# Optimization experiments

Measured on AMD Instinct MI355X. Metric: run time of the kernel, lower is better.

The kernel has to match this reference:

```python
import jax, jax.numpy as jnp
import numpy as np
import math

B, S, D, H, DH = 2, 4096, 1024, 16, 64
CHUNK, RNDS, NBUCK, MLP = 128, 2, 64, 4096


def setup_inputs() -> dict:
    key = jax.random.key(0)
    ks = jax.random.split(key, 8)
    return {
        "inputs": jax.random.normal(ks[0], (B, S, D), jnp.float32),
        "ln1_scale": jnp.ones((D,), jnp.float32),
        "ln1_bias": jnp.zeros((D,), jnp.float32),
        "w_qk": jax.random.normal(ks[1], (D, H, DH), jnp.float32) * 0.02,
        "w_v": jax.random.normal(ks[2], (D, H, DH), jnp.float32) * 0.02,
        "w_out": jax.random.normal(ks[3], (H, DH, D), jnp.float32) * 0.02,
        "rotations": jax.random.normal(ks[4], (DH, RNDS, NBUCK // 2), jnp.float32),
        "ln2_scale": jnp.ones((D,), jnp.float32),
        "ln2_bias": jnp.zeros((D,), jnp.float32),
        "w_mlp1": jax.random.normal(ks[5], (D, MLP), jnp.float32) * 0.02,
        "b_mlp1": jnp.zeros((MLP,), jnp.float32),
        "w_mlp2": jax.random.normal(ks[6], (MLP, D), jnp.float32) * 0.02,
        "b_mlp2": jnp.zeros((D,), jnp.float32),
    }


def _layer_norm(x, scale, bias):
    mu = x.mean(-1, keepdims=True)
    var = ((x - mu) ** 2).mean(-1, keepdims=True)
    return (x - mu) / jnp.sqrt(var + 1e-6) * scale + bias


def _attend_one(q, k, v, buckets):
    # q,k,v: [S,DH]; buckets: [S] int. Sort by bucket (stable via position tiebreak),
    # chunk, attend to own chunk + 1 before + 1 after (look_both_side).
    nC = S // CHUNK
    order = jnp.argsort(buckets * S + jnp.arange(S))  # [S]
    undo = jnp.argsort(order)
    sq = q[order].reshape(nC, CHUNK, DH)
    sk = k[order].reshape(nC, CHUNK, DH)
    sv = v[order].reshape(nC, CHUNK, DH)
    st = order.reshape(nC, CHUNK)  # original token positions
    look = lambda x: jnp.concatenate([x, jnp.roll(x, 1, axis=0), jnp.roll(x, -1, axis=0)], axis=1)
    bk, bv = look(sk), look(sv)
    bt = look(st[..., None])[..., 0]
    dots = jnp.einsum('nqd,nkd->nqk', sq, bk) / math.sqrt(DH)
    # self_mask: a token attends to itself only if nothing else is available
    dots = dots - 1e5 * (st[:, :, None] == bt[:, None, :]).astype(dots.dtype)
    slog = jax.nn.logsumexp(dots, axis=-1)           # [nC,CHUNK]
    o = jnp.einsum('nqk,nkd->nqd', jax.nn.softmax(dots, axis=-1), bv)
    return o.reshape(S, DH)[undo], slog.reshape(S)[undo]


def _lsh_attention(qk, v, rotations):
    # qk,v: [B,H,S,DH]; shared-QK Reformer attention; keys are length-normalized.
    xn = qk / (jnp.linalg.norm(qk, axis=-1, keepdims=True) + 1e-6)
    rot = jnp.einsum('bhsd,drm->bhrsm', xn, rotations)          # [B,H,R,S,NBUCK/2]
    buckets = jnp.argmax(jnp.concatenate([rot, -rot], -1), -1)  # [B,H,R,S]
    rep = lambda x: jnp.broadcast_to(x[:, :, None], (B, H, RNDS, S, DH)).reshape(-1, S, DH)
    o, slog = jax.vmap(_attend_one)(rep(qk), rep(xn), rep(v), buckets.reshape(-1, S))
    o = o.reshape(B, H, RNDS, S, DH)
    slog = slog.reshape(B, H, RNDS, S)
    w = jax.nn.softmax(slog, axis=2)  # combine hash rounds by their logsumexp weight
    return (o * w[..., None]).sum(axis=2)  # [B,H,S,DH]


def reference(inputs, ln1_scale, ln1_bias, w_qk, w_v, w_out, rotations,
              ln2_scale, ln2_bias, w_mlp1, b_mlp1, w_mlp2, b_mlp2):
    x = _layer_norm(inputs, ln1_scale, ln1_bias)
    qk = jnp.einsum('bsd,dhe->bhse', x, w_qk)
    v = jnp.einsum('bsd,dhe->bhse', x, w_v)
    att = _lsh_attention(qk, v, rotations)
    x2 = inputs + jnp.einsum('bhse,hed->bsd', att, w_out)
    y = _layer_norm(x2, ln2_scale, ln2_bias)
    y = jax.nn.gelu(y @ w_mlp1 + b_mlp1) @ w_mlp2 + b_mlp2
    return x2 + y
```

## Files before the change

kernel.cpp:

```cpp
#include <hip/hip_runtime.h>
#include <hip/hip_bf16.h>


typedef short short8 __attribute__((ext_vector_type(8)));
typedef float f32x4 __attribute__((ext_vector_type(4)));
typedef unsigned short us4 __attribute__((ext_vector_type(4)));

__device__ __forceinline__ unsigned short f2bf(float f) {
  unsigned u = __builtin_bit_cast(unsigned, f);
  u += 0x7FFFu + ((u >> 16) & 1u);
  return (unsigned short)(u >> 16);
}

__device__ __forceinline__ float bf2f(unsigned short u) {
  return __builtin_bit_cast(float, ((unsigned)u) << 16);
}

__device__ __forceinline__ float gelu_f(float x) {
  float y = 1.5957691216057308f * (x + 0.044715f * x * x * x);
  return x / (1.f + __expf(-y));
}

__device__ __forceinline__ void load_lds16(const void* g, void* l) {
  __builtin_amdgcn_global_load_lds(
      (const __attribute__((address_space(1))) unsigned int*)g,
      (__attribute__((address_space(3))) unsigned int*)l, 16, 0, 0);
}

__global__ __launch_bounds__(256) void transpose_cast(
    const float* __restrict__ in, unsigned short* __restrict__ out, int R,
    int C) {
  __shared__ float tile[32][33];
  int ctiles = C >> 5;
  int bx = blockIdx.x % ctiles;
  int by = blockIdx.x / ctiles;
  int tx = threadIdx.x & 31;
  int ty = threadIdx.x >> 5;
#pragma unroll
  for (int i = 0; i < 32; i += 8)
    tile[ty + i][tx] = in[(size_t)(by * 32 + ty + i) * C + bx * 32 + tx];
  __syncthreads();
#pragma unroll
  for (int i = 0; i < 32; i += 8)
    out[(size_t)(bx * 32 + ty + i) * R + by * 32 + tx] = f2bf(tile[tx][ty + i]);
}

__global__ __launch_bounds__(256) void ln_bf16(const float* __restrict__ x,
                                               const float* __restrict__ sc,
                                               const float* __restrict__ bi,
                                               unsigned short* __restrict__ y) {
  int row = blockIdx.x, tid = threadIdx.x, lane = tid & 63, wv = tid >> 6;
  const float* xr = x + (size_t)row * 1024;
  float4 v = *(const float4*)(xr + tid * 4);
  float s1 = v.x + v.y + v.z + v.w;
  float s2 = v.x * v.x + v.y * v.y + v.z * v.z + v.w * v.w;
#pragma unroll
  for (int o = 1; o < 64; o <<= 1) {
    s1 += __shfl_xor(s1, o);
    s2 += __shfl_xor(s2, o);
  }
  __shared__ float a1[4], a2[4];
  if (lane == 0) {
    a1[wv] = s1;
    a2[wv] = s2;
  }
  __syncthreads();
  s1 = a1[0] + a1[1] + a1[2] + a1[3];
  s2 = a2[0] + a2[1] + a2[2] + a2[3];
  float mu = s1 * (1.f / 1024.f);
  float var = s2 * (1.f / 1024.f) - mu * mu;
  float rs = rsqrtf(var + 1e-6f);
  int c = tid * 4;
  us4 o4;
  o4.x = f2bf((v.x - mu) * rs * sc[c + 0] + bi[c + 0]);
  o4.y = f2bf((v.y - mu) * rs * sc[c + 1] + bi[c + 1]);
  o4.z = f2bf((v.z - mu) * rs * sc[c + 2] + bi[c + 2]);
  o4.w = f2bf((v.w - mu) * rs * sc[c + 3] + bi[c + 3]);
  *(us4*)(y + (size_t)row * 1024 + c) = o4;
}

template <int EPI>
__global__ __launch_bounds__(256) void gemm_bt(
    const unsigned short* __restrict__ A, const unsigned short* __restrict__ Bt,
    const float* __restrict__ bias, const float* __restrict__ res,
    float* __restrict__ Cf, unsigned short* __restrict__ Cb, int M, int N,
    int K) {
  __shared__ unsigned short sA[2][128 * 64];
  __shared__ unsigned short sB[2][128 * 64];
  const int nbx = N / 128;
  const int nwg = gridDim.x;
  const int cpx = nwg >> 3;
  const int bid = blockIdx.x;
  const int swz = (bid & 7) * cpx + (bid >> 3);
  const int bx = swz % nbx;
  const int by = swz / nbx;
  const int tid = threadIdx.x;
  const int lane = tid & 63;
  const int wave = tid >> 6;
  const int wr = wave >> 1, wc = wave & 1;
  const int l15 = lane & 15;
  const int lhi = lane >> 4;

  const int srow = tid >> 3;
  const int sgl = (tid & 7) ^ (srow & 7);
  const unsigned short* Ag = A + (size_t)(by * 128 + srow) * K + sgl * 8;
  const unsigned short* Bg = Bt + (size_t)(bx * 128 + srow) * K + sgl * 8;

  f32x4 acc[4][4];
#pragma unroll
  for (int m = 0; m < 4; ++m)
#pragma unroll
    for (int n = 0; n < 4; ++n) {
      f32x4 z = {0.f, 0.f, 0.f, 0.f};
      acc[m][n] = z;
    }

  const int KT = K / 64;

  auto STAGE = [&](int ktile, int buf) {
    const unsigned short* As = Ag + (size_t)ktile * 64;
    const unsigned short* Bs = Bg + (size_t)ktile * 64;
#pragma unroll
    for (int i = 0; i < 4; ++i) {
      load_lds16(As + (size_t)i * 32 * K,
                 (char*)&sA[buf][0] + tid * 16 + i * 4096);
      load_lds16(Bs + (size_t)i * 32 * K,
                 (char*)&sB[buf][0] + tid * 16 + i * 4096);
    }
  };

  STAGE(0, 0);
  __syncthreads();

  int cur = 0;
  const int arow = wr * 64 + l15;
  const int brow = wc * 64 + l15;

  for (int kt = 0; kt < KT; ++kt) {
    if (kt + 1 < KT) STAGE(kt + 1, cur ^ 1);
#pragma unroll
    for (int ks = 0; ks < 2; ++ks) {
      const int koff = (((ks * 4 + lhi) ^ (l15 & 7)) << 3);
      short8 af[4], bfv[4];
#pragma unroll
      for (int m = 0; m < 4; ++m)
        af[m] = *(const short8*)&sA[cur][(arow + m * 16) * 64 + koff];
#pragma unroll
      for (int n = 0; n < 4; ++n)
        bfv[n] = *(const short8*)&sB[cur][(brow + n * 16) * 64 + koff];
#pragma unroll
      for (int m = 0; m < 4; ++m)
#pragma unroll
        for (int n = 0; n < 4; ++n)
          acc[m][n] = __builtin_amdgcn_mfma_f32_16x16x32_bf16(
              af[m], bfv[n], acc[m][n], 0, 0, 0);
    }
    __syncthreads();
    cur ^= 1;
  }

  const int r0 = by * 128 + wr * 64;
  const int c0 = bx * 128 + wc * 64;
#pragma unroll
  for (int m = 0; m < 4; ++m) {
#pragma unroll
    for (int n = 0; n < 4; ++n) {
#pragma unroll
      for (int i = 0; i < 4; ++i) {
        int rr = r0 + m * 16 + lhi * 4 + i;
        int cc = c0 + n * 16 + l15;
        float vacc = acc[m][n][i];
        if (EPI == 2) {
          float t = vacc + res[(size_t)rr * N + cc];
          if (bias != nullptr) t += bias[cc];
          Cf[(size_t)rr * N + cc] = t;
        }
      }
    }
  }
}

template <int EPI>
__global__ __launch_bounds__(512, 2) void gemm_8p(
    const unsigned short* __restrict__ A, const unsigned short* __restrict__ Bt,
    const float* __restrict__ bias, float* __restrict__ Cf,
    unsigned short* __restrict__ Cb, unsigned short* __restrict__ Cb2, int M,
    int N, int K) {
  __shared__ unsigned short sA[2][256 * 64];
  __shared__ unsigned short sB[2][256 * 64];
  const int nbx = N >> 8;
  const int nwg = gridDim.x;
  const int cpx = nwg >> 3;
  const int bid = blockIdx.x;
  const int swz = (bid & 7) * cpx + (bid >> 3);
  const int bx = swz % nbx;
  const int by = swz / nbx;
  const int tid = threadIdx.x;
  const int lane = tid & 63;
  const int wid = tid >> 6;
  const int wr = wid >> 2;
  const int wc = wid & 3;
  const int l15 = lane & 15;
  const int lhi = lane >> 4;

  const int sr = tid >> 3;
  const int sgl = (tid & 7) ^ (sr & 7);
  const unsigned short* Ab = A + ((size_t)(by * 256) + sr) * K + sgl * 8;
  const unsigned short* Bb = Bt + ((size_t)(bx * 256) + sr) * K + sgl * 8;

  f32x4 acc[8][4];
#pragma unroll
  for (int m = 0; m < 8; ++m)
#pragma unroll
    for (int n = 0; n < 4; ++n) {
      f32x4 z = {0.f, 0.f, 0.f, 0.f};
      acc[m][n] = z;
    }

  const int KT = K >> 6;

  auto ISSUE = [&](int mat, int half, int kt, int buf) {
    const unsigned short* src =
        (mat ? Bb : Ab) + (size_t)(half * 128) * K + kt * 64;
    char* d =
        (char*)(mat ? &sB[buf][0] : &sA[buf][0]) + half * 16384 + tid * 16;
    load_lds16(src, d);
    load_lds16(src + (size_t)64 * K, d + 8192);
  };

  auto rdA = [&](int m, int ks, int c) {
    int row = ((m & 4) << 5) + wr * 64 + ((m & 3) << 4) + l15;
    int pg = ((ks << 2) + lhi) ^ (l15 & 7);
    return *(const short8*)&sA[c][row * 64 + pg * 8];
  };
  auto rdB = [&](int n, int ks, int c) {
    int row = ((n & 2) << 6) + wc * 32 + ((n & 1) << 4) + l15;
    int pg = ((ks << 2) + lhi) ^ (l15 & 7);
    return *(const short8*)&sB[c][row * 64 + pg * 8];
  };

#define PRE_MFMA()                                   \
  __builtin_amdgcn_sched_barrier(0);                 \
  __builtin_amdgcn_s_barrier();                      \
  asm volatile("s_waitcnt lgkmcnt(0)" ::: "memory"); \
  __builtin_amdgcn_sched_barrier(0);                 \
  __builtin_amdgcn_s_setprio(1)
#define POST_MFMA()                \
  __builtin_amdgcn_s_setprio(0);   \
  __builtin_amdgcn_sched_barrier(0); \
  __builtin_amdgcn_s_barrier()

  ISSUE(0, 0, 0, 0);
  ISSUE(1, 0, 0, 0);
  ISSUE(0, 1, 0, 0);
  ISSUE(1, 1, 0, 0);
  asm volatile("s_waitcnt vmcnt(4)" ::: "memory");
  if (KT > 1) {
    ISSUE(0, 0, 1, 1);
    ISSUE(1, 0, 1, 1);
    ISSUE(0, 1, 1, 1);
  }
  asm volatile("s_waitcnt vmcnt(6)" ::: "memory");
  __builtin_amdgcn_sched_barrier(0);
  __builtin_amdgcn_s_barrier();

  for (int kt = 0; kt < KT; ++kt) {
    const int c = kt & 1;
    short8 a0[4][2], a1[4][2], b0[2][2], b1[2][2];

#pragma unroll
    for (int m = 0; m < 4; ++m)
#pragma unroll
      for (int ks = 0; ks < 2; ++ks) a0[m][ks] = rdA(m, ks, c);
#pragma unroll
    for (int n = 0; n < 2; ++n)
#pragma unroll
      for (int ks = 0; ks < 2; ++ks) b0[n][ks] = rdB(n, ks, c);
    if (kt + 1 < KT) ISSUE(1, 1, kt + 1, c ^ 1);
    PRE_MFMA();
#pragma unroll
    for (int m = 0; m < 4; ++m)
#pragma unroll
      for (int n = 0; n < 2; ++n)
#pragma unroll
        for (int ks = 0; ks < 2; ++ks)
          acc[m][n] = __builtin_amdgcn_mfma_f32_16x16x32_bf16(
              a0[m][ks], b0[n][ks], acc[m][n], 0, 0, 0);
    POST_MFMA();

#pragma unroll
    for (int m = 0; m < 4; ++m)
#pragma unroll
      for (int ks = 0; ks < 2; ++ks) a1[m][ks] = rdA(4 + m, ks, c);
    if (kt + 2 < KT) ISSUE(0, 0, kt + 2, c);
    PRE_MFMA();
#pragma unroll
    for (int m = 0; m < 4; ++m)
#pragma unroll
      for (int n = 0; n < 2; ++n)
#pragma unroll
        for (int ks = 0; ks < 2; ++ks)
          acc[4 + m][n] = __builtin_amdgcn_mfma_f32_16x16x32_bf16(
              a1[m][ks], b0[n][ks], acc[4 + m][n], 0, 0, 0);
    POST_MFMA();

#pragma unroll
    for (int n = 0; n < 2; ++n)
#pragma unroll
      for (int ks = 0; ks < 2; ++ks) b1[n][ks] = rdB(2 + n, ks, c);
    if (kt + 2 < KT) ISSUE(1, 0, kt + 2, c);
    PRE_MFMA();
#pragma unroll
    for (int m = 0; m < 4; ++m)
#pragma unroll
      for (int n = 0; n < 2; ++n)
#pragma unroll
        for (int ks = 0; ks < 2; ++ks)
          acc[4 + m][2 + n] = __builtin_amdgcn_mfma_f32_16x16x32_bf16(
              a1[m][ks], b1[n][ks], acc[4 + m][2 + n], 0, 0, 0);
    POST_MFMA();

    if (kt + 2 < KT) ISSUE(0, 1, kt + 2, c);
    __builtin_amdgcn_s_setprio(1);
#pragma unroll
    for (int m = 0; m < 4; ++m)
#pragma unroll
      for (int n = 0; n < 2; ++n)
#pragma unroll
        for (int ks = 0; ks < 2; ++ks)
          acc[m][2 + n] = __builtin_amdgcn_mfma_f32_16x16x32_bf16(
              a0[m][ks], b1[n][ks], acc[m][2 + n], 0, 0, 0);
    __builtin_amdgcn_s_setprio(0);
    if (kt + 1 < KT) {
      if (kt + 2 < KT) {
        asm volatile("s_waitcnt vmcnt(6)" ::: "memory");
      } else {
        asm volatile("s_waitcnt vmcnt(0)" ::: "memory");
      }
      __builtin_amdgcn_sched_barrier(0);
      __builtin_amdgcn_s_barrier();
    }
  }
#undef PRE_MFMA
#undef POST_MFMA

  const int r0 = by * 256 + wr * 64;
  const int c0 = bx * 256 + wc * 32;
#pragma unroll
  for (int m = 0; m < 8; ++m) {
    const int rb = r0 + ((m & 4) << 5) + ((m & 3) << 4) + lhi * 4;
#pragma unroll
    for (int n = 0; n < 4; ++n) {
      const int cc = c0 + ((n & 2) << 6) + ((n & 1) << 4) + l15;
#pragma unroll
      for (int i = 0; i < 4; ++i) {
        const int rr = rb + i;
        float vacc = acc[m][n][i];
        if (EPI == 1) {
          Cb[(size_t)rr * N + cc] = f2bf(gelu_f(vacc + bias[cc]));
        } else if (EPI == 5) {
          if (cc < 1024) {
            Cf[(size_t)rr * 1024 + cc] = vacc;
            Cb[(size_t)rr * 1024 + cc] = f2bf(vacc);
          } else {
            Cb2[(size_t)rr * 1024 + (cc - 1024)] = f2bf(vacc);
          }
        }
      }
    }
  }
}

__global__ __launch_bounds__(256) void bucket_kernel(
    const float* __restrict__ qk, const float* __restrict__ rot,
    unsigned short* __restrict__ knb, int* __restrict__ buckets) {
  __shared__ float rotl[64 * 64];
  __shared__ float xnl[4][64];
  int tid = threadIdx.x, lane = tid & 63, wv = tid >> 6;
  for (int i = tid; i < 4096; i += 256) rotl[i] = rot[i];
  __syncthreads();
  for (int it = 0; it < 8; ++it) {
    int g = (it * 4096 + blockIdx.x) * 4 + wv;
    int bh = g >> 12;
    int s = g & 4095;
    int b = bh >> 4, h = bh & 15;
    size_t rowoff = (size_t)(b * 4096 + s) * 1024 + h * 64;
    float x = qk[rowoff + lane];
    float ss = x * x;
#pragma unroll
    for (int o = 1; o < 64; o <<= 1) ss += __shfl_xor(ss, o);
    float rn = 1.f / (sqrtf(ss) + 1e-6f);
    float xn = x * rn;
    knb[rowoff + lane] = f2bf(xn);
    xnl[wv][lane] = xn;
    __syncthreads();
    int r_ = lane >> 5, m_ = lane & 31;
    float a = 0.f;
#pragma unroll 16
    for (int d = 0; d < 64; ++d) a += xnl[wv][d] * rotl[d * 64 + r_ * 32 + m_];
    float bv;
    int bi;
    if (a >= 0.f) {
      bv = a;
      bi = m_;
    } else {
      bv = -a;
      bi = m_ + 32;
    }
#pragma unroll
    for (int o = 16; o >= 1; o >>= 1) {
      float ov = __shfl_xor(bv, o);
      int oi = __shfl_xor(bi, o);
      if (ov > bv || (ov == bv && oi < bi)) {
        bv = ov;
        bi = oi;
      }
    }
    if (m_ == 0) buckets[((size_t)bh * 2 + r_) * 4096 + s] = bi;
    __syncthreads();
  }
}

#define HSTR 65

__global__ __launch_bounds__(256) void sort_kernel(
    const int* __restrict__ buckets, int* __restrict__ order) {
  __shared__ unsigned int hist[256 * HSTR];
  __shared__ unsigned int bucketStart[64];
  const int bhr = blockIdx.x;
  const int t = threadIdx.x;
  const int* bk = buckets + (size_t)bhr * 4096;

  unsigned int* hrow = &hist[t * HSTR];
#pragma unroll
  for (int b = 0; b < 64; ++b) hrow[b] = 0u;

  int bks[16];
  {
    const int4* bp = (const int4*)(bk + t * 16);
#pragma unroll
    for (int j4 = 0; j4 < 4; ++j4) {
      int4 v = bp[j4];
      bks[j4 * 4 + 0] = v.x;
      bks[j4 * 4 + 1] = v.y;
      bks[j4 * 4 + 2] = v.z;
      bks[j4 * 4 + 3] = v.w;
    }
  }
#pragma unroll
  for (int j = 0; j < 16; ++j) hrow[bks[j]]++;
  __syncthreads();

  if (t < 64) {
    unsigned int acc = 0;
    for (int t2 = 0; t2 < 256; ++t2) {
      unsigned int c = hist[t2 * HSTR + t];
      hist[t2 * HSTR + t] = acc;
      acc += c;
    }
    bucketStart[t] = acc;
  }
  __syncthreads();
  if (t == 0) {
    unsigned int acc = 0;
    for (int b = 0; b < 64; ++b) {
      unsigned int c = bucketStart[b];
      bucketStart[b] = acc;
      acc += c;
    }
  }
  __syncthreads();

  int* op = order + (size_t)bhr * 4096;
#pragma unroll
  for (int j = 0; j < 16; ++j) {
    int b = bks[j];
    unsigned int pos = bucketStart[b] + hrow[b];
    hrow[b]++;
    op[pos] = t * 16 + j;
  }
}

#define KSTR 72
#define PSTR 136

__global__ __launch_bounds__(256, 2) void lsh_attn_mfma(
    const unsigned short* __restrict__ qb, const unsigned short* __restrict__ knb,
    const unsigned short* __restrict__ vb, const int* __restrict__ order,
    unsigned short* __restrict__ ob, float* __restrict__ slog) {
  __shared__ unsigned short Kls[128 * KSTR];
  __shared__ unsigned short Vt[64 * PSTR];
  __shared__ unsigned short Pls[4][32 * PSTR];
  __shared__ int qtokL[128];
  __shared__ int btok[128];

  const int bid = blockIdx.x;
  const int swz = (bid & 7) * 256 + (bid >> 3);
  const int c = swz & 31;
  const int bhr = swz >> 5;
  const int bh = bhr >> 1;
  const int h = bh & 15, b = bh >> 4;
  const int* ord = order + (size_t)bhr * 4096;
  const int tid = threadIdx.x, lane = tid & 63, wv = tid >> 6;
  const int l15 = lane & 15, lhi = lane >> 4;

  if (tid < 128) qtokL[tid] = ord[c * 128 + tid];
  __syncthreads();

  short8 qf[2][2];
#pragma unroll
  for (int mt = 0; mt < 2; ++mt) {
#pragma unroll
    for (int ks = 0; ks < 2; ++ks) {
      int tok = qtokL[wv * 32 + mt * 16 + l15];
      qf[mt][ks] = *(const short8*)(qb + (size_t)(b * 4096 + tok) * 1024 +
                                    h * 64 + ks * 32 + lhi * 8);
    }
  }

  float mrun[2][4], lrun[2][4];
  f32x4 oacc[2][4];
#pragma unroll
  for (int mt = 0; mt < 2; ++mt)
#pragma unroll
    for (int i = 0; i < 4; ++i) {
      mrun[mt][i] = -1e30f;
      lrun[mt][i] = 0.f;
    }
#pragma unroll
  for (int mt = 0; mt < 2; ++mt)
#pragma unroll
    for (int n = 0; n < 4; ++n) {
      f32x4 z = {0.f, 0.f, 0.f, 0.f};
      oacc[mt][n] = z;
    }

  for (int st = 0; st < 3; ++st) {
    int kc = (st == 0) ? c : (st == 1) ? ((c + 31) & 31) : ((c + 1) & 31);
    __syncthreads();
    {
      int row = tid >> 1, half = tid & 1;
      int ktok = ord[kc * 128 + row];
      if (half == 0) btok[row] = ktok;
      size_t rowoff = (size_t)(b * 4096 + ktok) * 1024 + h * 64 + half * 32;
      const short8* kp = (const short8*)(knb + rowoff);
      const short8* vp = (const short8*)(vb + rowoff);
#pragma unroll
      for (int i = 0; i < 4; ++i)
        *(short8*)&Kls[row * KSTR + half * 32 + i * 8] = kp[i];
#pragma unroll
      for (int i = 0; i < 4; ++i) {
        short8 vw = vp[i];
        int d0 = half * 32 + i * 8;
#pragma unroll
        for (int j = 0; j < 8; ++j)
          Vt[(d0 + j) * PSTR + row] = (unsigned short)vw[j];
      }
    }
    __syncthreads();

    f32x4 sacc[2][8];
#pragma unroll
    for (int mt = 0; mt < 2; ++mt)
#pragma unroll
      for (int n = 0; n < 8; ++n) {
        f32x4 z = {0.f, 0.f, 0.f, 0.f};
        sacc[mt][n] = z;
      }
#pragma unroll
    for (int ks = 0; ks < 2; ++ks) {
      short8 kf[8];
#pragma unroll
      for (int n = 0; n < 8; ++n)
        kf[n] = *(const short8*)&Kls[(n * 16 + l15) * KSTR + ks * 32 + lhi * 8];
#pragma unroll
      for (int mt = 0; mt < 2; ++mt)
#pragma unroll
        for (int n = 0; n < 8; ++n)
          sacc[mt][n] = __builtin_amdgcn_mfma_f32_16x16x32_bf16(
              qf[mt][ks], kf[n], sacc[mt][n], 0, 0, 0);
    }

    int ktA[8];
#pragma unroll
    for (int n = 0; n < 8; ++n) ktA[n] = btok[n * 16 + l15];
#pragma unroll
    for (int mt = 0; mt < 2; ++mt) {
#pragma unroll
      for (int i = 0; i < 4; ++i) {
        int qrow = wv * 32 + mt * 16 + lhi * 4 + i;
        int qt = qtokL[qrow];
        float sv[8];
        float mx = -1e30f;
#pragma unroll
        for (int n = 0; n < 8; ++n) {
          float s = sacc[mt][n][i] * 0.125f;
          if (ktA[n] == qt) s -= 1e5f;
          sv[n] = s;
          mx = fmaxf(mx, s);
        }
#pragma unroll
        for (int d = 1; d < 16; d <<= 1) mx = fmaxf(mx, __shfl_xor(mx, d));
        float mold = mrun[mt][i];
        float mnew = fmaxf(mold, mx);
        float scl = __expf(mold - mnew);
        lrun[mt][i] *= scl;
#pragma unroll
        for (int n = 0; n < 4; ++n) oacc[mt][n][i] *= scl;
        float ps = 0.f;
#pragma unroll
        for (int n = 0; n < 8; ++n) {
          float p = __expf(sv[n] - mnew);
          ps += p;
          Pls[wv][(mt * 16 + lhi * 4 + i) * PSTR + n * 16 + l15] = f2bf(p);
        }
#pragma unroll
        for (int d = 1; d < 16; d <<= 1) ps += __shfl_xor(ps, d);
        lrun[mt][i] = lrun[mt][i] + ps;
        mrun[mt][i] = mnew;
      }
    }

#pragma unroll
    for (int ks = 0; ks < 4; ++ks) {
      short8 pf[2];
#pragma unroll
      for (int mt = 0; mt < 2; ++mt)
        pf[mt] =
            *(const short8*)&Pls[wv][(mt * 16 + l15) * PSTR + ks * 32 + lhi * 8];
      short8 vfr[4];
#pragma unroll
      for (int n = 0; n < 4; ++n)
        vfr[n] = *(const short8*)&Vt[(n * 16 + l15) * PSTR + ks * 32 + lhi * 8];
#pragma unroll
      for (int mt = 0; mt < 2; ++mt)
#pragma unroll
        for (int n = 0; n < 4; ++n)
          oacc[mt][n] = __builtin_amdgcn_mfma_f32_16x16x32_bf16(
              pf[mt], vfr[n], oacc[mt][n], 0, 0, 0);
    }
  }

#pragma unroll
  for (int mt = 0; mt < 2; ++mt) {
#pragma unroll
    for (int i = 0; i < 4; ++i) {
      int qrow = wv * 32 + mt * 16 + lhi * 4 + i;
      int tok = qtokL[qrow];
      float l = lrun[mt][i];
      float invl = 1.f / l;
      if (l15 == 0) slog[(size_t)bhr * 4096 + tok] = logf(l) + mrun[mt][i];
      unsigned short* orow = ob + ((size_t)bhr * 4096 + tok) * 64;
#pragma unroll
      for (int n = 0; n < 4; ++n)
        orow[n * 16 + l15] = f2bf(oacc[mt][n][i] * invl);
    }
  }
}

__global__ __launch_bounds__(256) void combine_rounds(
    const unsigned short* __restrict__ ob, const float* __restrict__ slog,
    unsigned short* __restrict__ att) {
  int g = blockIdx.x * 4 + (threadIdx.x >> 6);
  int lane = threadIdx.x & 63;
  int h = g & 15;
  int bs = g >> 4;
  int b = bs >> 12;
  int s = bs & 4095;
  size_t base = ((size_t)(b * 16 + h) * 2) * 4096 + s;
  size_t i0 = base;
  size_t i1 = base + 4096;
  float s0 = slog[i0], s1 = slog[i1];
  float mx = fmaxf(s0, s1);
  float e0 = __expf(s0 - mx), e1 = __expf(s1 - mx);
  float w0 = e0 / (e0 + e1);
  float w1 = 1.f - w0;
  float v0 = bf2f(ob[i0 * 64 + lane]);
  float v1 = bf2f(ob[i1 * 64 + lane]);
  att[(size_t)bs * 1024 + h * 64 + lane] = f2bf(w0 * v0 + w1 * v1);
}

extern "C" void kernel_launch(void* const* d_in, const int* in_sizes, int n_in,
                              void* d_out, int out_size, void* d_ws,
                              size_t ws_size, hipStream_t stream) {
  const float* inputs = (const float*)d_in[0];
  const float* ln1s = (const float*)d_in[1];
  const float* ln1b = (const float*)d_in[2];
  const float* wqk = (const float*)d_in[3];
  const float* wv = (const float*)d_in[4];
  const float* wout = (const float*)d_in[5];
  const float* rot = (const float*)d_in[6];
  const float* ln2s = (const float*)d_in[7];
  const float* ln2b = (const float*)d_in[8];
  const float* wm1 = (const float*)d_in[9];
  const float* bm1 = (const float*)d_in[10];
  const float* wm2 = (const float*)d_in[11];
  const float* bm2 = (const float*)d_in[12];

  char* w = (char*)d_ws;
  auto alloc = [&](size_t bytes) {
    char* p = w;
    w += (bytes + 255) & ~(size_t)255;
    return p;
  };
  unsigned short* wqkv_bt = (unsigned short*)alloc(2048ull * 1024 * 2);
  unsigned short* wout_bt = (unsigned short*)alloc(1024ull * 1024 * 2);
  unsigned short* wm1_bt = (unsigned short*)alloc(4096ull * 1024 * 2);
  unsigned short* wm2_bt = (unsigned short*)alloc(1024ull * 4096 * 2);
  unsigned short* bufA = (unsigned short*)alloc(8192ull * 1024 * 2);
  float* qkf = (float*)alloc(8192ull * 1024 * 4);
  unsigned short* qb = (unsigned short*)alloc(8192ull * 1024 * 2);
  unsigned short* knb = (unsigned short*)alloc(8192ull * 1024 * 2);
  unsigned short* vb = (unsigned short*)alloc(8192ull * 1024 * 2);
  int* buckets = (int*)alloc(64ull * 4096 * 4);
  int* order = (int*)alloc(64ull * 4096 * 4);
  unsigned short* big =
      (unsigned short*)alloc(8192ull * 4096 * 2);
  float* slogb = (float*)alloc(64ull * 4096 * 4);
  float* x2 = qkf;
  unsigned short* obuf = big;
  unsigned short* h1 = big;

  transpose_cast<<<32 * 32, 256, 0, stream>>>(wqk, wqkv_bt, 1024, 1024);
  transpose_cast<<<32 * 32, 256, 0, stream>>>(wv, wqkv_bt + 1024ull * 1024,
                                              1024, 1024);
  transpose_cast<<<32 * 32, 256, 0, stream>>>(wout, wout_bt, 1024, 1024);
  transpose_cast<<<32 * 128, 256, 0, stream>>>(wm1, wm1_bt, 1024, 4096);
  transpose_cast<<<128 * 32, 256, 0, stream>>>(wm2, wm2_bt, 4096, 1024);

  ln_bf16<<<8192, 256, 0, stream>>>(inputs, ln1s, ln1b, bufA);

  gemm_8p<5><<<32 * 8, 512, 0, stream>>>(bufA, wqkv_bt, nullptr, qkf, qb, vb,
                                         8192, 2048, 1024);

  bucket_kernel<<<4096, 256, 0, stream>>>(qkf, rot, knb, buckets);
  sort_kernel<<<64, 256, 0, stream>>>(buckets, order);
  lsh_attn_mfma<<<2048, 256, 0, stream>>>(qb, knb, vb, order, obuf, slogb);
  combine_rounds<<<32768, 256, 0, stream>>>(obuf, slogb, bufA);

  gemm_bt<2><<<64 * 8, 256, 0, stream>>>(bufA, wout_bt, nullptr, inputs, x2,
                                         nullptr, 8192, 1024, 1024);
  ln_bf16<<<8192, 256, 0, stream>>>(x2, ln2s, ln2b, bufA);
  gemm_8p<1><<<32 * 16, 512, 0, stream>>>(bufA, wm1_bt, bm1, nullptr, h1,
                                          nullptr, 8192, 4096, 1024);
  gemm_bt<2><<<64 * 8, 256, 0, stream>>>(h1, wm2_bt, bm2, x2, (float*)d_out,
                                         nullptr, 8192, 1024, 4096);
}
```

Baseline: 471.4 us.

## Replace simple 128x128 GEMM with pipelined 256x128 8-wave GEMM for out-proj and MLP2

Replaces the basic double-buffered 128x128 gemm_bt used for the attention output projection and second MLP matmul with a new 512-thread 256x128 tile kernel. The new kernel uses the same phased schedule as gemm_8p: split LDS loads, explicit vmcnt waits, barriers and setprio around the MFMA blocks. It aims to overlap global loads with MFMA and reuse more data per tile. In exchange it launches only 256 workgroups, which may leave compute units underused on the N=1024 shapes.

```diff
diff --git a/kernel.cpp b/kernel.cpp
--- a/kernel.cpp
+++ b/kernel.cpp
@@ -79,106 +79,16 @@
   *(us4*)(y + (size_t)row * 1024 + c) = o4;
 }
 
-template <int EPI>
-__global__ __launch_bounds__(256) void gemm_bt(
-    const unsigned short* __restrict__ A, const unsigned short* __restrict__ Bt,
-    const float* __restrict__ bias, const float* __restrict__ res,
-    float* __restrict__ Cf, unsigned short* __restrict__ Cb, int M, int N,
-    int K) {
-  __shared__ unsigned short sA[2][128 * 64];
-  __shared__ unsigned short sB[2][128 * 64];
-  const int nbx = N / 128;
-  const int nwg = gridDim.x;
-  const int cpx = nwg >> 3;
-  const int bid = blockIdx.x;
-  const int swz = (bid & 7) * cpx + (bid >> 3);
-  const int bx = swz % nbx;
-  const int by = swz / nbx;
-  const int tid = threadIdx.x;
-  const int lane = tid & 63;
-  const int wave = tid >> 6;
-  const int wr = wave >> 1, wc = wave & 1;
-  const int l15 = lane & 15;
-  const int lhi = lane >> 4;
-
-  const int srow = tid >> 3;
-  const int sgl = (tid & 7) ^ (srow & 7);
-  const unsigned short* Ag = A + (size_t)(by * 128 + srow) * K + sgl * 8;
-  const unsigned short* Bg = Bt + (size_t)(bx * 128 + srow) * K + sgl * 8;
-
-  f32x4 acc[4][4];
-#pragma unroll
-  for (int m = 0; m < 4; ++m)
-#pragma unroll
-    for (int n = 0; n < 4; ++n) {
-      f32x4 z = {0.f, 0.f, 0.f, 0.f};
-      acc[m][n] = z;
-    }
-
-  const int KT = K / 64;
-
-  auto STAGE = [&](int ktile, int buf) {
-    const unsigned short* As = Ag + (size_t)ktile * 64;
-    const unsigned short* Bs = Bg + (size_t)ktile * 64;
-#pragma unroll
-    for (int i = 0; i < 4; ++i) {
-      load_lds16(As + (size_t)i * 32 * K,
-                 (char*)&sA[buf][0] + tid * 16 + i * 4096);
-      load_lds16(Bs + (size_t)i * 32 * K,
-                 (char*)&sB[buf][0] + tid * 16 + i * 4096);
-    }
-  };
-
-  STAGE(0, 0);
-  __syncthreads();
-
-  int cur = 0;
-  const int arow = wr * 64 + l15;
-  const int brow = wc * 64 + l15;
-
-  for (int kt = 0; kt < KT; ++kt) {
-    if (kt + 1 < KT) STAGE(kt + 1, cur ^ 1);
-#pragma unroll
-    for (int ks = 0; ks < 2; ++ks) {
-      const int koff = (((ks * 4 + lhi) ^ (l15 & 7)) << 3);
-      short8 af[4], bfv[4];
-#pragma unroll
-      for (int m = 0; m < 4; ++m)
-        af[m] = *(const short8*)&sA[cur][(arow + m * 16) * 64 + koff];
-#pragma unroll
-      for (int n = 0; n < 4; ++n)
-        bfv[n] = *(const short8*)&sB[cur][(brow + n * 16) * 64 + koff];
-#pragma unroll
-      for (int m = 0; m < 4; ++m)
-#pragma unroll
-        for (int n = 0; n < 4; ++n)
-          acc[m][n] = __builtin_amdgcn_mfma_f32_16x16x32_bf16(
-              af[m], bfv[n], acc[m][n], 0, 0, 0);
-    }
-    __syncthreads();
-    cur ^= 1;
-  }
-
-  const int r0 = by * 128 + wr * 64;
-  const int c0 = bx * 128 + wc * 64;
-#pragma unroll
-  for (int m = 0; m < 4; ++m) {
-#pragma unroll
-    for (int n = 0; n < 4; ++n) {
-#pragma unroll
-      for (int i = 0; i < 4; ++i) {
-        int rr = r0 + m * 16 + lhi * 4 + i;
-        int cc = c0 + n * 16 + l15;
-        float vacc = acc[m][n][i];
-        if (EPI == 2) {
-          float t = vacc + res[(size_t)rr * N + cc];
-          if (bias != nullptr) t += bias[cc];
-          Cf[(size_t)rr * N + cc] = t;
-        }
-      }
-    }
-  }
-}
+#define PRE_MFMA()                                   \
+  __builtin_amdgcn_sched_barrier(0);                 \
+  __builtin_amdgcn_s_barrier();                      \
+  asm volatile("s_waitcnt lgkmcnt(0)" ::: "memory"); \
+  __builtin_amdgcn_sched_barrier(0);                 \
+  __builtin_amdgcn_s_setprio(1)
+#define POST_MFMA()                  \
+  __builtin_amdgcn_s_setprio(0);     \
+  __builtin_amdgcn_sched_barrier(0); \
+  __builtin_amdgcn_s_barrier()
 
 template <int EPI>
 __global__ __launch_bounds__(512, 2) void gemm_8p(
@@ -239,17 +149,6 @@
     return *(const short8*)&sB[c][row * 64 + pg * 8];
   };
 
-#define PRE_MFMA()                                   \
-  __builtin_amdgcn_sched_barrier(0);                 \
-  __builtin_amdgcn_s_barrier();                      \
-  asm volatile("s_waitcnt lgkmcnt(0)" ::: "memory"); \
-  __builtin_amdgcn_sched_barrier(0);                 \
-  __builtin_amdgcn_s_setprio(1)
-#define POST_MFMA()                \
-  __builtin_amdgcn_s_setprio(0);   \
-  __builtin_amdgcn_sched_barrier(0); \
-  __builtin_amdgcn_s_barrier()
-
   ISSUE(0, 0, 0, 0);
   ISSUE(1, 0, 0, 0);
   ISSUE(0, 1, 0, 0);
@@ -341,8 +240,6 @@
       __builtin_amdgcn_s_barrier();
     }
   }
-#undef PRE_MFMA
-#undef POST_MFMA
 
   const int r0 = by * 256 + wr * 64;
   const int c0 = bx * 256 + wc * 32;
@@ -370,6 +267,157 @@
     }
   }
 }
+
+template <int EPI>
+__global__ __launch_bounds__(512, 2) void gemm_8pn(
+    const unsigned short* __restrict__ A, const unsigned short* __restrict__ Bt,
+    const float* __restrict__ bias, const float* __restrict__ res,
+    float* __restrict__ Cf, int M, int N, int K) {
+  __shared__ unsigned short sA[2][256 * 64];
+  __shared__ unsigned short sB[2][128 * 64];
+  const int nbx = N >> 7;
+  const int nwg = gridDim.x;
+  const int cpx = nwg >> 3;
+  const int bid = blockIdx.x;
+  const int swz = (bid & 7) * cpx + (bid >> 3);
+  const int bx = swz % nbx;
+  const int by = swz / nbx;
+  const int tid = threadIdx.x;
+  const int lane = tid & 63;
+  const int wid = tid >> 6;
+  const int wr = wid >> 1;
+  const int wc = wid & 1;
+  const int l15 = lane & 15;
+  const int lhi = lane >> 4;
+
+  const int sr = tid >> 3;
+  const int sgl = (tid & 7) ^ (sr & 7);
+  const unsigned short* Ab = A + ((size_t)(by * 256) + sr) * K + sgl * 8;
+  const unsigned short* Bb = Bt + ((size_t)(bx * 128) + sr) * K + sgl * 8;
+
+  f32x4 acc[4][4];
+#pragma unroll
+  for (int m = 0; m < 4; ++m)
+#pragma unroll
+    for (int n = 0; n < 4; ++n) {
+      f32x4 z = {0.f, 0.f, 0.f, 0.f};
+      acc[m][n] = z;
+    }
+
+  const int KT = K >> 6;
+
+  auto ISSA = [&](int half, int kt, int buf) {
+    const unsigned short* src = Ab + (size_t)(half * 128) * K + kt * 64;
+    char* d = (char*)&sA[buf][0] + half * 16384 + tid * 16;
+    load_lds16(src, d);
+    load_lds16(src + (size_t)64 * K, d + 8192);
+  };
+  auto ISSB = [&](int half, int kt, int buf) {
+    const unsigned short* src = Bb + (size_t)(half * 64) * K + kt * 64;
+    char* d = (char*)&sB[buf][0] + half * 8192 + tid * 16;
+    load_lds16(src, d);
+  };
+
+  auto rdA = [&](int m, int ks, int c) {
+    int row = wr * 64 + (m << 4) + l15;
+    int pg = ((ks << 2) + lhi) ^ (l15 & 7);
+    return *(const short8*)&sA[c][row * 64 + pg * 8];
+  };
+  auto rdB = [&](int n, int ks, int c) {
+    int row = ((n & 2) << 5) + wc * 32 + ((n & 1) << 4) + l15;
+    int pg = ((ks << 2) + lhi) ^ (l15 & 7);
+    return *(const short8*)&sB[c][row * 64 + pg * 8];
+  };
+
+  ISSA(0, 0, 0);
+  ISSB(0, 0, 0);
+  ISSA(1, 0, 0);
+  ISSB(1, 0, 0);
+  if (KT > 1) {
+    ISSA(0, 1, 1);
+    ISSB(0, 1, 1);
+    ISSA(1, 1, 1);
+  }
+  asm volatile("s_waitcnt vmcnt(5)" ::: "memory");
+  __builtin_amdgcn_sched_barrier(0);
+  __builtin_amdgcn_s_barrier();
+
+  for (int kt = 0; kt < KT; ++kt) {
+    const int c = kt & 1;
+    short8 a[4][2], b0[2][2], b1[2][2];
+
+#pragma unroll
+    for (int m = 0; m < 4; ++m)
+#pragma unroll
+      for (int ks = 0; ks < 2; ++ks) a[m][ks] = rdA(m, ks, c);
+#pragma unroll
+    for (int n = 0; n < 2; ++n)
+#pragma unroll
+      for (int ks = 0; ks < 2; ++ks) b0[n][ks] = rdB(n, ks, c);
+    if (kt + 1 < KT) ISSB(1, kt + 1, c ^ 1);
+    PRE_MFMA();
+#pragma unroll
+    for (int m = 0; m < 4; ++m)
+#pragma unroll
+      for (int n = 0; n < 2; ++n)
+#pragma unroll
+        for (int ks = 0; ks < 2; ++ks)
+          acc[m][n] = __builtin_amdgcn_mfma_f32_16x16x32_bf16(
+              a[m][ks], b0[n][ks], acc[m][n], 0, 0, 0);
+    POST_MFMA();
+
+#pragma unroll
+    for (int n = 0; n < 2; ++n)
+#pragma unroll
+      for (int ks = 0; ks < 2; ++ks) b1[n][ks] = rdB(2 + n, ks, c);
+    if (kt + 2 < KT) {
+      ISSA(0, kt + 2, c);
+      ISSB(0, kt + 2, c);
+      ISSA(1, kt + 2, c);
+    }
+    PRE_MFMA();
+#pragma unroll
+    for (int m = 0; m < 4; ++m)
+#pragma unroll
+      for (int n = 0; n < 2; ++n)
+#pragma unroll
+        for (int ks = 0; ks < 2; ++ks)
+          acc[m][2 + n] = __builtin_amdgcn_mfma_f32_16x16x32_bf16(
+              a[m][ks], b1[n][ks], acc[m][2 + n], 0, 0, 0);
+    POST_MFMA();
+
+    if (kt + 1 < KT) {
+      if (kt + 2 < KT) {
+        asm volatile("s_waitcnt vmcnt(5)" ::: "memory");
+      } else {
+        asm volatile("s_waitcnt vmcnt(0)" ::: "memory");
+      }
+      __builtin_amdgcn_sched_barrier(0);
+      __builtin_amdgcn_s_barrier();
+    }
+  }
+
+  const int r0 = by * 256 + wr * 64;
+  const int c0 = bx * 128 + wc * 32;
+#pragma unroll
+  for (int m = 0; m < 4; ++m) {
+    const int rb = r0 + (m << 4) + lhi * 4;
+#pragma unroll
+    for (int n = 0; n < 4; ++n) {
+      const int cc = c0 + ((n & 2) << 5) + ((n & 1) << 4) + l15;
+#pragma unroll
+      for (int i = 0; i < 4; ++i) {
+        const int rr = rb + i;
+        float t = acc[m][n][i] + res[(size_t)rr * N + cc];
+        if (bias != nullptr) t += bias[cc];
+        Cf[(size_t)rr * N + cc] = t;
+      }
+    }
+  }
+}
+
+#undef PRE_MFMA
+#undef POST_MFMA
 
 __global__ __launch_bounds__(256) void bucket_kernel(
     const float* __restrict__ qk, const float* __restrict__ rot,
@@ -738,11 +786,11 @@
   lsh_attn_mfma<<<2048, 256, 0, stream>>>(qb, knb, vb, order, obuf, slogb);
   combine_rounds<<<32768, 256, 0, stream>>>(obuf, slogb, bufA);
 
-  gemm_bt<2><<<64 * 8, 256, 0, stream>>>(bufA, wout_bt, nullptr, inputs, x2,
-                                         nullptr, 8192, 1024, 1024);
+  gemm_8pn<2><<<32 * 8, 512, 0, stream>>>(bufA, wout_bt, nullptr, inputs, x2,
+                                          8192, 1024, 1024);
   ln_bf16<<<8192, 256, 0, stream>>>(x2, ln2s, ln2b, bufA);
   gemm_8p<1><<<32 * 16, 512, 0, stream>>>(bufA, wm1_bt, bm1, nullptr, h1,
                                           nullptr, 8192, 4096, 1024);
-  gemm_bt<2><<<64 * 8, 256, 0, stream>>>(h1, wm2_bt, bm2, x2, (float*)d_out,
-                                         nullptr, 8192, 1024, 4096);
-}
+  gemm_8pn<2><<<32 * 8, 512, 0, stream>>>(h1, wm2_bt, bm2, x2, (float*)d_out,
+                                          8192, 1024, 4096);
+}
```

Result: no change. 471.0 us (-0.1%).

## Replace residual GEMM with 256x128 tile kernel and drop fp32 QK output

Applied to the files above, without the earlier changes.

The residual-epilogue GEMMs (out-projection and MLP2) move to a new kernel with a 256x128 tile and K-step 32, giving each wave an 8x4 MFMA accumulator block for more reuse and launching half as many workgroups. The QKV GEMM no longer writes an fp32 copy of qk, and the bucket kernel now reads the bf16 qk, cutting about 32MB of writes and reads. The trade-off is that bucket hashing uses bf16-rounded qk, which can flip bucket assignments near ties. The larger accumulator also raises register pressure and lowers occupancy.

```diff
diff --git a/kernel.cpp b/kernel.cpp
--- a/kernel.cpp
+++ b/kernel.cpp
@@ -79,106 +79,16 @@
   *(us4*)(y + (size_t)row * 1024 + c) = o4;
 }
 
-template <int EPI>
-__global__ __launch_bounds__(256) void gemm_bt(
-    const unsigned short* __restrict__ A, const unsigned short* __restrict__ Bt,
-    const float* __restrict__ bias, const float* __restrict__ res,
-    float* __restrict__ Cf, unsigned short* __restrict__ Cb, int M, int N,
-    int K) {
-  __shared__ unsigned short sA[2][128 * 64];
-  __shared__ unsigned short sB[2][128 * 64];
-  const int nbx = N / 128;
-  const int nwg = gridDim.x;
-  const int cpx = nwg >> 3;
-  const int bid = blockIdx.x;
-  const int swz = (bid & 7) * cpx + (bid >> 3);
-  const int bx = swz % nbx;
-  const int by = swz / nbx;
-  const int tid = threadIdx.x;
-  const int lane = tid & 63;
-  const int wave = tid >> 6;
-  const int wr = wave >> 1, wc = wave & 1;
-  const int l15 = lane & 15;
-  const int lhi = lane >> 4;
-
-  const int srow = tid >> 3;
-  const int sgl = (tid & 7) ^ (srow & 7);
-  const unsigned short* Ag = A + (size_t)(by * 128 + srow) * K + sgl * 8;
-  const unsigned short* Bg = Bt + (size_t)(bx * 128 + srow) * K + sgl * 8;
-
-  f32x4 acc[4][4];
-#pragma unroll
-  for (int m = 0; m < 4; ++m)
-#pragma unroll
-    for (int n = 0; n < 4; ++n) {
-      f32x4 z = {0.f, 0.f, 0.f, 0.f};
-      acc[m][n] = z;
-    }
-
-  const int KT = K / 64;
-
-  auto STAGE = [&](int ktile, int buf) {
-    const unsigned short* As = Ag + (size_t)ktile * 64;
-    const unsigned short* Bs = Bg + (size_t)ktile * 64;
-#pragma unroll
-    for (int i = 0; i < 4; ++i) {
-      load_lds16(As + (size_t)i * 32 * K,
-                 (char*)&sA[buf][0] + tid * 16 + i * 4096);
-      load_lds16(Bs + (size_t)i * 32 * K,
-                 (char*)&sB[buf][0] + tid * 16 + i * 4096);
-    }
-  };
-
-  STAGE(0, 0);
-  __syncthreads();
-
-  int cur = 0;
-  const int arow = wr * 64 + l15;
-  const int brow = wc * 64 + l15;
-
-  for (int kt = 0; kt < KT; ++kt) {
-    if (kt + 1 < KT) STAGE(kt + 1, cur ^ 1);
-#pragma unroll
-    for (int ks = 0; ks < 2; ++ks) {
-      const int koff = (((ks * 4 + lhi) ^ (l15 & 7)) << 3);
-      short8 af[4], bfv[4];
-#pragma unroll
-      for (int m = 0; m < 4; ++m)
-        af[m] = *(const short8*)&sA[cur][(arow + m * 16) * 64 + koff];
-#pragma unroll
-      for (int n = 0; n < 4; ++n)
-        bfv[n] = *(const short8*)&sB[cur][(brow + n * 16) * 64 + koff];
-#pragma unroll
-      for (int m = 0; m < 4; ++m)
-#pragma unroll
-        for (int n = 0; n < 4; ++n)
-          acc[m][n] = __builtin_amdgcn_mfma_f32_16x16x32_bf16(
-              af[m], bfv[n], acc[m][n], 0, 0, 0);
-    }
-    __syncthreads();
-    cur ^= 1;
-  }
-
-  const int r0 = by * 128 + wr * 64;
-  const int c0 = bx * 128 + wc * 64;
-#pragma unroll
-  for (int m = 0; m < 4; ++m) {
-#pragma unroll
-    for (int n = 0; n < 4; ++n) {
-#pragma unroll
-      for (int i = 0; i < 4; ++i) {
-        int rr = r0 + m * 16 + lhi * 4 + i;
-        int cc = c0 + n * 16 + l15;
-        float vacc = acc[m][n][i];
-        if (EPI == 2) {
-          float t = vacc + res[(size_t)rr * N + cc];
-          if (bias != nullptr) t += bias[cc];
-          Cf[(size_t)rr * N + cc] = t;
-        }
-      }
-    }
-  }
-}
+#define PRE_MFMA()                                   \
+  __builtin_amdgcn_sched_barrier(0);                 \
+  __builtin_amdgcn_s_barrier();                      \
+  asm volatile("s_waitcnt lgkmcnt(0)" ::: "memory"); \
+  __builtin_amdgcn_sched_barrier(0);                 \
+  __builtin_amdgcn_s_setprio(1)
+#define POST_MFMA()                  \
+  __builtin_amdgcn_s_setprio(0);     \
+  __builtin_amdgcn_sched_barrier(0); \
+  __builtin_amdgcn_s_barrier()
 
 template <int EPI>
 __global__ __launch_bounds__(512, 2) void gemm_8p(
@@ -239,17 +149,6 @@
     return *(const short8*)&sB[c][row * 64 + pg * 8];
   };
 
-#define PRE_MFMA()                                   \
-  __builtin_amdgcn_sched_barrier(0);                 \
-  __builtin_amdgcn_s_barrier();                      \
-  asm volatile("s_waitcnt lgkmcnt(0)" ::: "memory"); \
-  __builtin_amdgcn_sched_barrier(0);                 \
-  __builtin_amdgcn_s_setprio(1)
-#define POST_MFMA()                \
-  __builtin_amdgcn_s_setprio(0);   \
-  __builtin_amdgcn_sched_barrier(0); \
-  __builtin_amdgcn_s_barrier()
-
   ISSUE(0, 0, 0, 0);
   ISSUE(1, 0, 0, 0);
   ISSUE(0, 1, 0, 0);
@@ -341,8 +240,6 @@
       __builtin_amdgcn_s_barrier();
     }
   }
-#undef PRE_MFMA
-#undef POST_MFMA
 
   const int r0 = by * 256 + wr * 64;
   const int c0 = bx * 256 + wc * 32;
@@ -360,7 +257,6 @@
           Cb[(size_t)rr * N + cc] = f2bf(gelu_f(vacc + bias[cc]));
         } else if (EPI == 5) {
           if (cc < 1024) {
-            Cf[(size_t)rr * 1024 + cc] = vacc;
             Cb[(size_t)rr * 1024 + cc] = f2bf(vacc);
           } else {
             Cb2[(size_t)rr * 1024 + (cc - 1024)] = f2bf(vacc);
@@ -371,8 +267,108 @@
   }
 }
 
+#undef PRE_MFMA
+#undef POST_MFMA
+
+template <int EPI>
+__global__ __launch_bounds__(256) void gemm_w(
+    const unsigned short* __restrict__ A, const unsigned short* __restrict__ Bt,
+    const float* __restrict__ bias, const float* __restrict__ res,
+    float* __restrict__ Cf, int M, int N, int K) {
+  __shared__ unsigned short sA[2][256 * 32];
+  __shared__ unsigned short sB[2][128 * 32];
+  const int nbx = N >> 7;
+  const int nwg = gridDim.x;
+  const int cpx = nwg >> 3;
+  const int bid = blockIdx.x;
+  const int swz = (bid & 7) * cpx + (bid >> 3);
+  const int bx = swz % nbx;
+  const int by = swz / nbx;
+  const int tid = threadIdx.x;
+  const int lane = tid & 63;
+  const int wid = tid >> 6;
+  const int wr = wid >> 1;
+  const int wc = wid & 1;
+  const int l15 = lane & 15;
+  const int lhi = lane >> 4;
+
+  const int srow = tid >> 2;
+  const int sgl = (tid & 3) ^ ((srow >> 1) & 3);
+  const unsigned short* Ag = A + (size_t)(by * 256 + srow) * K + sgl * 8;
+  const unsigned short* Bg = Bt + (size_t)(bx * 128 + srow) * K + sgl * 8;
+
+  f32x4 acc[8][4];
+#pragma unroll
+  for (int m = 0; m < 8; ++m)
+#pragma unroll
+    for (int n = 0; n < 4; ++n) {
+      f32x4 z = {0.f, 0.f, 0.f, 0.f};
+      acc[m][n] = z;
+    }
+
+  const int KT = K >> 5;
+
+  auto STAGE = [&](int ktile, int buf) {
+    const unsigned short* As = Ag + (size_t)ktile * 32;
+    const unsigned short* Bs = Bg + (size_t)ktile * 32;
+#pragma unroll
+    for (int i = 0; i < 4; ++i)
+      load_lds16(As + (size_t)i * 64 * K,
+                 (char*)&sA[buf][0] + tid * 16 + i * 4096);
+#pragma unroll
+    for (int i = 0; i < 2; ++i)
+      load_lds16(Bs + (size_t)i * 64 * K,
+                 (char*)&sB[buf][0] + tid * 16 + i * 4096);
+  };
+
+  STAGE(0, 0);
+  __syncthreads();
+
+  int cur = 0;
+  const int arow0 = wr * 128;
+  const int brow0 = wc * 64;
+  const int koff = (lhi ^ ((l15 >> 1) & 3)) * 8;
+
+  for (int kt = 0; kt < KT; ++kt) {
+    if (kt + 1 < KT) STAGE(kt + 1, cur ^ 1);
+    short8 af[8], bfv[4];
+#pragma unroll
+    for (int m = 0; m < 8; ++m)
+      af[m] = *(const short8*)&sA[cur][(arow0 + m * 16 + l15) * 32 + koff];
+#pragma unroll
+    for (int n = 0; n < 4; ++n)
+      bfv[n] = *(const short8*)&sB[cur][(brow0 + n * 16 + l15) * 32 + koff];
+#pragma unroll
+    for (int m = 0; m < 8; ++m)
+#pragma unroll
+      for (int n = 0; n < 4; ++n)
+        acc[m][n] = __builtin_amdgcn_mfma_f32_16x16x32_bf16(af[m], bfv[n],
+                                                            acc[m][n], 0, 0, 0);
+    __syncthreads();
+    cur ^= 1;
+  }
+
+  const int r0 = by * 256 + wr * 128;
+  const int c0 = bx * 128 + wc * 64;
+#pragma unroll
+  for (int m = 0; m < 8; ++m) {
+    const int rb = r0 + m * 16 + lhi * 4;
+#pragma unroll
+    for (int n = 0; n < 4; ++n) {
+      const int cc = c0 + n * 16 + l15;
+#pragma unroll
+      for (int i = 0; i < 4; ++i) {
+        const int rr = rb + i;
+        float t = acc[m][n][i] + res[(size_t)rr * N + cc];
+        if (bias != nullptr) t += bias[cc];
+        Cf[(size_t)rr * N + cc] = t;
+      }
+    }
+  }
+}
+
 __global__ __launch_bounds__(256) void bucket_kernel(
-    const float* __restrict__ qk, const float* __restrict__ rot,
+    const unsigned short* __restrict__ qk, const float* __restrict__ rot,
     unsigned short* __restrict__ knb, int* __restrict__ buckets) {
   __shared__ float rotl[64 * 64];
   __shared__ float xnl[4][64];
@@ -385,7 +381,7 @@
     int s = g & 4095;
     int b = bh >> 4, h = bh & 15;
     size_t rowoff = (size_t)(b * 4096 + s) * 1024 + h * 64;
-    float x = qk[rowoff + lane];
+    float x = bf2f(qk[rowoff + lane]);
     float ss = x * x;
 #pragma unroll
     for (int o = 1; o < 64; o <<= 1) ss += __shfl_xor(ss, o);
@@ -708,7 +704,7 @@
   unsigned short* wm1_bt = (unsigned short*)alloc(4096ull * 1024 * 2);
   unsigned short* wm2_bt = (unsigned short*)alloc(1024ull * 4096 * 2);
   unsigned short* bufA = (unsigned short*)alloc(8192ull * 1024 * 2);
-  float* qkf = (float*)alloc(8192ull * 1024 * 4);
+  float* x2 = (float*)alloc(8192ull * 1024 * 4);
   unsigned short* qb = (unsigned short*)alloc(8192ull * 1024 * 2);
   unsigned short* knb = (unsigned short*)alloc(8192ull * 1024 * 2);
   unsigned short* vb = (unsigned short*)alloc(8192ull * 1024 * 2);
@@ -717,7 +713,6 @@
   unsigned short* big =
       (unsigned short*)alloc(8192ull * 4096 * 2);
   float* slogb = (float*)alloc(64ull * 4096 * 4);
-  float* x2 = qkf;
   unsigned short* obuf = big;
   unsigned short* h1 = big;
 
@@ -730,19 +725,19 @@
 
   ln_bf16<<<8192, 256, 0, stream>>>(inputs, ln1s, ln1b, bufA);
 
-  gemm_8p<5><<<32 * 8, 512, 0, stream>>>(bufA, wqkv_bt, nullptr, qkf, qb, vb,
-                                         8192, 2048, 1024);
-
-  bucket_kernel<<<4096, 256, 0, stream>>>(qkf, rot, knb, buckets);
+  gemm_8p<5><<<32 * 8, 512, 0, stream>>>(bufA, wqkv_bt, nullptr, nullptr, qb,
+                                         vb, 8192, 2048, 1024);
+
+  bucket_kernel<<<4096, 256, 0, stream>>>(qb, rot, knb, buckets);
   sort_kernel<<<64, 256, 0, stream>>>(buckets, order);
   lsh_attn_mfma<<<2048, 256, 0, stream>>>(qb, knb, vb, order, obuf, slogb);
   combine_rounds<<<32768, 256, 0, stream>>>(obuf, slogb, bufA);
 
-  gemm_bt<2><<<64 * 8, 256, 0, stream>>>(bufA, wout_bt, nullptr, inputs, x2,
-                                         nullptr, 8192, 1024, 1024);
+  gemm_w<2><<<32 * 8, 256, 0, stream>>>(bufA, wout_bt, nullptr, inputs, x2,
+                                        8192, 1024, 1024);
   ln_bf16<<<8192, 256, 0, stream>>>(x2, ln2s, ln2b, bufA);
   gemm_8p<1><<<32 * 16, 512, 0, stream>>>(bufA, wm1_bt, bm1, nullptr, h1,
                                           nullptr, 8192, 4096, 1024);
-  gemm_bt<2><<<64 * 8, 256, 0, stream>>>(h1, wm2_bt, bm2, x2, (float*)d_out,
-                                         nullptr, 8192, 1024, 4096);
-}
+  gemm_w<2><<<32 * 8, 256, 0, stream>>>(h1, wm2_bt, bm2, x2, (float*)d_out,
+                                        8192, 1024, 4096);
+}
```

Result: slower. 557.3 us (+18.2%).
